# Performance work log

Measured on AMD Instinct MI355X. Metric: run time of the kernel, lower is better.

The kernel has to match this reference:

```python
import jax, jax.numpy as jnp
import numpy as np

NEG_SLOPE = 0.2  # neg_slope init kwarg


def _segment_softmax(logits, seg, n):
    # numerically stable softmax over edges grouped by destination node
    m = jax.ops.segment_max(logits, seg, num_segments=n)          # [N,H]
    e = jnp.exp(logits - m[seg])                                   # [E,H]
    s = jax.ops.segment_sum(e, seg, num_segments=n)                # [N,H]
    return e / (s[seg] + 1e-16)


def _gat_conv(x, src, dst, W, att_src, att_dst, b, n):
    # PyG GATConv (add_self_loops already applied to src/dst), dropout off (eval)
    H, C = att_src.shape
    h = (x @ W).reshape(n, H, C)                                   # [N,H,C]
    a_src = jnp.einsum('nhc,hc->nh', h, att_src)                   # [N,H]
    a_dst = jnp.einsum('nhc,hc->nh', h, att_dst)                   # [N,H]
    logits = jax.nn.leaky_relu(a_src[src] + a_dst[dst], NEG_SLOPE)  # [E,H]
    alpha = _segment_softmax(logits, dst, n)                       # [E,H]
    msg = h[src] * alpha[:, :, None]                               # [E,H,C]
    out = jax.ops.segment_sum(msg, dst, num_segments=n)            # [N,H,C]
    return out.reshape(n, H * C) + b


def setup_inputs() -> dict:
    key = jax.random.key(0)
    ks = jax.random.split(key, 11)
    NU, NI = 10000, 100000
    N = NU + NI
    E = 1_000_000
    IN, HID, HEADS, OUT = 64, 64, 4, 64
    s = 0.1
    return {
        'edge_index': jax.random.randint(ks[0], (2, E), 0, N, dtype=jnp.int64)
            if jax.config.jax_enable_x64 else jax.random.randint(ks[0], (2, E), 0, N),
        'emb_user': jax.random.normal(ks[1], (NU, IN), jnp.float32) * s,
        'emb_item': jax.random.normal(ks[2], (NI, IN), jnp.float32) * s,
        'W1': jax.random.normal(ks[3], (IN, HEADS * HID), jnp.float32) * s,
        'att_src1': jax.random.normal(ks[4], (HEADS, HID), jnp.float32) * s,
        'att_dst1': jax.random.normal(ks[5], (HEADS, HID), jnp.float32) * s,
        'b1': jnp.zeros((HEADS * HID,), jnp.float32),
        'W2': jax.random.normal(ks[6], (HEADS * HID, OUT), jnp.float32) * s,
        'att_src2': jax.random.normal(ks[7], (1, OUT), jnp.float32) * s,
        'att_dst2': jax.random.normal(ks[8], (1, OUT), jnp.float32) * s,
        'b2': jnp.zeros((OUT,), jnp.float32),
    }


def reference(edge_index, emb_user, emb_item, W1, att_src1, att_dst1, b1,
              W2, att_src2, att_dst2, b2):
    NU = emb_user.shape[0]
    N = NU + emb_item.shape[0]
    x = jnp.concatenate([emb_user, emb_item], axis=0)              # [N,IN]
    # GATConv adds self-loops by default
    loops = jnp.arange(N, dtype=edge_index.dtype)
    src = jnp.concatenate([edge_index[0], loops])
    dst = jnp.concatenate([edge_index[1], loops])
    # dropout layers are identity in eval mode
    x = _gat_conv(x, src, dst, W1, att_src1, att_dst1, b1, N)      # [N,HEADS*HID]
    x = jax.nn.elu(x)
    x = _gat_conv(x, src, dst, W2, att_src2, att_dst2, b2, N)      # [N,OUT]
    return x[:NU], x[NU:]
```

## Files before the change

kernel.cpp:

```cpp
#include <hip/hip_runtime.h>
#include <math.h>


typedef float f32x4 __attribute__((ext_vector_type(4)));
typedef short s16x8 __attribute__((ext_vector_type(8)));

#define CHUNK 4096
#define CAPB 6400
#define PADM 1536
#define CAPT (CAPB + PADM)
#define G2PAD 264

static __device__ __forceinline__ short f2bf(float f) {
    unsigned u = __builtin_bit_cast(unsigned, f);
    u = (u + 0x7fff + ((u >> 16) & 1)) >> 16;
    return (short)u;
}
static __device__ __forceinline__ float bf2f(unsigned short u) {
    unsigned v = ((unsigned)u) << 16;
    return __builtin_bit_cast(float, v);
}


__global__ __launch_bounds__(256) void bin_kernel(
    const int* __restrict__ ei, int E, int ET, int* __restrict__ acur,
    unsigned long long* __restrict__ staging) {
    __shared__ unsigned long long eds[CHUNK];
    __shared__ int cnt[256], delta[256], cur[256];
    int t = threadIdx.x;
    cnt[t] = 0;
    __syncthreads();
    int c0 = blockIdx.x * CHUNK;
#pragma unroll
    for (int i = t; i < CHUNK; i += 256) {
        int e = c0 + i;
        unsigned long long v = ~0ull;
        if (e < ET) {
            int s, d;
            if (e < E) { s = ei[e]; d = ei[E + e]; } else { s = e - E; d = e - E; }
            v = ((unsigned long long)(unsigned)d << 32) | (unsigned)s;
            atomicAdd(&cnt[d >> 9], 1);
        }
        eds[i] = v;
    }
    __syncthreads();
    if (t < 64) {
        int loc[4], run = 0;
#pragma unroll
        for (int j = 0; j < 4; ++j) { int v = cnt[t * 4 + j]; loc[j] = run; run += v; }
        int inc = run;
#pragma unroll
        for (int off = 1; off < 64; off <<= 1) {
            int u = __shfl_up(inc, off);
            if (t >= off) inc += u;
        }
        int excl = inc - run;
#pragma unroll
        for (int j = 0; j < 4; ++j) {
            int b = t * 4 + j;
            int lofs = excl + loc[j];
            int c = cnt[b];
            int g = (c > 0) ? atomicAdd(&acur[b], c) : 0;
            delta[b] = b * CAPB + g - lofs;
            cur[b] = lofs;
        }
    }
    __syncthreads();
    for (int i = t; i < CHUNK; i += 256) {
        unsigned long long v = eds[i];
        if (v == ~0ull) continue;
        int b = (int)(v >> 32) >> 9;
        int p = atomicAdd(&cur[b], 1);
        int idx = delta[b] + p;
        if (idx < (b + 1) * CAPB) staging[idx] = v;
    }
}

__global__ __launch_bounds__(256) void bucket_scan_kernel(
    const int* __restrict__ acur, int* __restrict__ bbase, int NB) {
    __shared__ int sc[256];
    int t = threadIdx.x;
    int v = 0;
    if (t < NB) {
        int c = min(acur[t], CAPB);
        v = ((c + 3) & ~3) + PADM;
    }
    sc[t] = v;
    __syncthreads();
    if (t == 0) {
        int run = 0;
        for (int i = 0; i < NB; ++i) { int x = sc[i]; sc[i] = run; run += x; }
    }
    __syncthreads();
    if (t < NB) bbase[t] = sc[t];
}

__global__ __launch_bounds__(256) void bucket_build_kernel(
    const unsigned long long* __restrict__ staging, const int* __restrict__ acur,
    const int* __restrict__ bbase, const float* __restrict__ as1e,
    const float* __restrict__ ad1e, int* __restrict__ offs, int* __restrict__ ends,
    int* __restrict__ csr, int* __restrict__ dstA, float* __restrict__ wts1T,
    int N, int ETp, int NB) {
    __shared__ int src_s[CAPT];
    __shared__ unsigned short ln_s[CAPT];
    __shared__ float adl[512 * 8];
    __shared__ int cnt[512];
    __shared__ int lofs[512];
    __shared__ int tot4_s;
    int b = blockIdx.x;
    int t = threadIdx.x;
    int n0 = b << 9;
    int nn = min(512, N - n0);
    int tot = min(acur[b], CAPB);
    for (int i = t; i < nn * 8; i += 256) adl[i] = ad1e[(size_t)n0 * 8 + i];
    for (int i = t; i < 512; i += 256) cnt[i] = 0;
    for (int i = t; i < CAPT; i += 256) src_s[i] = -1;
    __syncthreads();
    const unsigned long long* sp = staging + (size_t)b * CAPB;
    for (int i = t; i < tot; i += 256)
        atomicAdd(&cnt[(int)(sp[i] >> 32) - n0], 1);
    __syncthreads();
    if (t < 64) {
        int loc[8];
        int run = 0;
#pragma unroll
        for (int j = 0; j < 8; ++j) {
            int v = (cnt[t * 8 + j] + 3) & ~3;
            loc[j] = run;
            run += v;
        }
        int inc = run;
#pragma unroll
        for (int off = 1; off < 64; off <<= 1) {
            int u = __shfl_up(inc, off);
            if (t >= off) inc += u;
        }
        int excl = inc - run;
#pragma unroll
        for (int j = 0; j < 8; ++j) lofs[t * 8 + j] = excl + loc[j];
        if (t == 63) tot4_s = inc;
    }
    __syncthreads();
    int base = bbase[b];
    int tot4 = tot4_s;
    for (int i = t; i < nn; i += 256) {
        int beg = base + lofs[i];
        offs[n0 + i] = beg;
        ends[n0 + i] = beg + ((cnt[i] + 3) & ~3);
    }
    if (b == NB - 1 && t == 0) offs[N] = base + tot4;
    __syncthreads();
    for (int i = t; i < 512; i += 256) cnt[i] = 0;
    __syncthreads();
    for (int i = t; i < tot; i += 256) {
        unsigned long long v = sp[i];
        int s = (int)(v & 0xffffffffu);
        int ln = (int)(v >> 32) - n0;
        int p = lofs[ln] + atomicAdd(&cnt[ln], 1);
        src_s[p] = s;
        ln_s[p] = (unsigned short)ln;
    }
    __syncthreads();
    for (int i = t; i < tot4; i += 256) {
        int s = src_s[i];
        if (s < 0) {
            csr[base + i] = 0;
            dstA[base + i] = -1;
            wts1T[(size_t)0 * ETp + base + i] = 0.f;
            wts1T[(size_t)1 * ETp + base + i] = 0.f;
            wts1T[(size_t)2 * ETp + base + i] = 0.f;
            wts1T[(size_t)3 * ETp + base + i] = 0.f;
        } else {
            int ln = ln_s[i];
            csr[base + i] = s;
            dstA[base + i] = n0 + ln;
            const float4* ap = reinterpret_cast<const float4*>(as1e + (size_t)s * 8);
            float4 a0 = ap[0], a1 = ap[1];
            const float* dl = adl + ln * 8;
            float wA, wB;
            wA = a0.x * dl[0]; wB = a0.y * dl[1];
            wts1T[(size_t)0 * ETp + base + i] = (wA >= 1.f) ? wA : wB;
            wA = a0.z * dl[2]; wB = a0.w * dl[3];
            wts1T[(size_t)1 * ETp + base + i] = (wA >= 1.f) ? wA : wB;
            wA = a1.x * dl[4]; wB = a1.y * dl[5];
            wts1T[(size_t)2 * ETp + base + i] = (wA >= 1.f) ? wA : wB;
            wA = a1.z * dl[6]; wB = a1.w * dl[7];
            wts1T[(size_t)3 * ETp + base + i] = (wA >= 1.f) ? wA : wB;
        }
    }
}

__global__ void edge_w2_kernel(const int* __restrict__ csr,
                               const int* __restrict__ dstA,
                               const float* __restrict__ as2e,
                               const float* __restrict__ ad2e,
                               float* __restrict__ wts2, int ETp) {
    int p = blockIdx.x * blockDim.x + threadIdx.x;
    if (p >= ETp) return;
    int d = dstA[p];
    if (d < 0) { wts2[p] = 0.f; return; }
    int s = csr[p];
    float2 ae = *reinterpret_cast<const float2*>(as2e + (size_t)s * 2);
    float2 de = *reinterpret_cast<const float2*>(ad2e + (size_t)d * 2);
    float wA = ae.x * de.x, wB = ae.y * de.y;
    wts2[p] = (wA >= 1.f) ? wA : wB;
}

__global__ void prep_attv_kernel(const float* __restrict__ W1,
                                 const float* __restrict__ attS1,
                                 const float* __restrict__ attD1,
                                 const float* __restrict__ W2,
                                 const float* __restrict__ attS2,
                                 const float* __restrict__ attD2,
                                 float* __restrict__ attv1s, float* __restrict__ attv1d,
                                 float* __restrict__ attv2s, float* __restrict__ attv2d) {
    int t = threadIdx.x;
    {
        int k = t >> 2, h = t & 3;
        float ss = 0.f, sd = 0.f;
        for (int c = 0; c < 64; ++c) {
            float w = W1[k * 256 + h * 64 + c];
            ss += w * attS1[h * 64 + c];
            sd += w * attD1[h * 64 + c];
        }
        attv1s[k * 4 + h] = ss;
        attv1d[k * 4 + h] = sd;
    }
    {
        float ss = 0.f, sd = 0.f;
        for (int c = 0; c < 64; ++c) {
            float w = W2[t * 64 + c];
            ss += w * attS2[c];
            sd += w * attD2[c];
        }
        attv2s[t] = ss;
        attv2d[t] = sd;
    }
}

__global__ __launch_bounds__(256) void cast_att_kernel(
    const float* __restrict__ xu, const float* __restrict__ xi, int NU, int N,
    const float* __restrict__ attv1s, const float* __restrict__ attv1d,
    unsigned short* __restrict__ xb, float* __restrict__ as1e,
    float* __restrict__ ad1e) {
    int t = threadIdx.x;
    int wv = t >> 6, l = t & 63, l15 = l & 15, lg = l >> 4;

    s16x8 Bfr[2];
#pragma unroll
    for (int ks = 0; ks < 2; ++ks) {
        s16x8 f;
#pragma unroll
        for (int j = 0; j < 8; ++j) {
            int k = ks * 32 + lg * 8 + j;
            float v = 0.f;
            if (l15 < 4) v = attv1s[k * 4 + l15];
            else if (l15 < 8) v = attv1d[k * 4 + (l15 - 4)];
            f[j] = f2bf(v);
        }
        Bfr[ks] = f;
    }

    int ntile = (N + 15) >> 4;
    int wid = blockIdx.x * 4 + wv;
    int stride = gridDim.x * 4;
    for (int tile = wid; tile < ntile; tile += stride) {
        int rbase = tile * 16;
        int arow = rbase + l15;
        bool valid = (arow < N);
        if (!valid) arow = N - 1;
        const float* xp = (arow < NU) ? (xu + (size_t)arow * 64)
                                      : (xi + (size_t)(arow - NU) * 64);
        s16x8 Afr[2];
#pragma unroll
        for (int ks = 0; ks < 2; ++ks) {
            const float4* p = reinterpret_cast<const float4*>(xp + ks * 32 + lg * 8);
            float4 v0 = p[0];
            float4 v1 = p[1];
            s16x8 f;
            f[0] = f2bf(v0.x); f[1] = f2bf(v0.y); f[2] = f2bf(v0.z); f[3] = f2bf(v0.w);
            f[4] = f2bf(v1.x); f[5] = f2bf(v1.y); f[6] = f2bf(v1.z); f[7] = f2bf(v1.w);
            Afr[ks] = f;
            if (valid)
                *reinterpret_cast<s16x8*>(xb + (size_t)arow * 64 + ks * 32 + lg * 8) = f;
        }
        f32x4 acc = (f32x4){0.f, 0.f, 0.f, 0.f};
        acc = __builtin_amdgcn_mfma_f32_16x16x32_bf16(Afr[0], Bfr[0], acc, 0, 0, 0);
        acc = __builtin_amdgcn_mfma_f32_16x16x32_bf16(Afr[1], Bfr[1], acc, 0, 0, 0);
        if (l15 < 8) {
            float* dst = (l15 < 4) ? as1e : ad1e;
            int h = l15 & 3;
#pragma unroll
            for (int i = 0; i < 4; ++i) {
                int r = rbase + lg * 4 + i;
                if (r < N) {
                    float s = acc[i];
                    dst[(size_t)r * 8 + h * 2 + 0] = __expf(s);
                    dst[(size_t)r * 8 + h * 2 + 1] = __expf(0.2f * s);
                }
            }
        }
    }
}

__global__ __launch_bounds__(256) void agg1_kernel(
    const unsigned short* __restrict__ xb, const float* __restrict__ wts1T,
    const int* __restrict__ offs, const int* __restrict__ ends,
    const int* __restrict__ csr, unsigned short* __restrict__ yb, int N, int ETp) {
    int wv = threadIdx.x >> 6, lane = threadIdx.x & 63;
    int n = __builtin_amdgcn_readfirstlane(blockIdx.x * 4 + wv);
    if (n >= N) return;
    int h = lane >> 4, c4 = (lane & 15) * 4;
    int beg = offs[n], end = ends[n];
    const float* wp = wts1T + (size_t)h * ETp;
    float ss = 0.f, a0 = 0.f, a1 = 0.f, a2 = 0.f, a3 = 0.f;

    f32x4 wC = *reinterpret_cast<const f32x4*>(wp + beg);
    ushort4 rC[4];
#pragma unroll
    for (int j = 0; j < 4; ++j) {
        int sj = __builtin_amdgcn_readfirstlane(csr[beg + j]);
        rC[j] = *reinterpret_cast<const ushort4*>(xb + (size_t)sj * 64 + c4);
    }
    for (int o = beg; o < end; o += 4) {
        int oN = o + 4;
        f32x4 wNv;
        ushort4 rN[4];
        if (oN < end) {
            wNv = *reinterpret_cast<const f32x4*>(wp + oN);
#pragma unroll
            for (int j = 0; j < 4; ++j) {
                int sj = __builtin_amdgcn_readfirstlane(csr[oN + j]);
                rN[j] = *reinterpret_cast<const ushort4*>(xb + (size_t)sj * 64 + c4);
            }
        }
#pragma unroll
        for (int j = 0; j < 4; ++j) {
            float w = wC[j];
            ss += w;
            a0 += w * bf2f(rC[j].x);
            a1 += w * bf2f(rC[j].y);
            a2 += w * bf2f(rC[j].z);
            a3 += w * bf2f(rC[j].w);
        }
        wC = wNv;
#pragma unroll
        for (int j = 0; j < 4; ++j) rC[j] = rN[j];
    }
    float inv = 1.f / (ss + 1e-16f);
    ushort4 ov;
    ov.x = (unsigned short)f2bf(a0 * inv);
    ov.y = (unsigned short)f2bf(a1 * inv);
    ov.z = (unsigned short)f2bf(a2 * inv);
    ov.w = (unsigned short)f2bf(a3 * inv);
    *reinterpret_cast<ushort4*>(yb + (size_t)n * 256 + h * 64 + c4) = ov;
}

__global__ __launch_bounds__(256) void gemm_mid_mfma(
    const unsigned short* __restrict__ yb, int N, const float* __restrict__ W1,
    const float* __restrict__ b1, const float* __restrict__ attv2s,
    const float* __restrict__ attv2d, unsigned short* __restrict__ x2,
    float* __restrict__ as2e, float* __restrict__ ad2e) {
    __shared__ float part_s[16][4];
    __shared__ float part_d[16][4];
    int t = threadIdx.x;
    int wv = t >> 6;
    int l = t & 63;
    int l15 = l & 15;
    int lg = l >> 4;

    s16x8 Bfr[4][2];
#pragma unroll
    for (int c = 0; c < 4; ++c)
#pragma unroll
        for (int ks = 0; ks < 2; ++ks) {
            s16x8 f;
#pragma unroll
            for (int j = 0; j < 8; ++j)
                f[j] = f2bf(W1[(size_t)(ks * 32 + lg * 8 + j) * 256 + (wv * 4 + c) * 16 + l15]);
            Bfr[c][ks] = f;
        }
    float bv[4], avs[4], avd[4];
#pragma unroll
    for (int c = 0; c < 4; ++c) {
        int col = (wv * 4 + c) * 16 + l15;
        bv[c] = b1[col];
        avs[c] = attv2s[col];
        avd[c] = attv2d[col];
    }

    int ntile = (N + 15) >> 4;
    for (int tile = blockIdx.x; tile < ntile; tile += gridDim.x) {
        int rbase = tile * 16;
        int arow = rbase + l15;
        if (arow >= N) arow = N - 1;
        const unsigned short* yp = yb + (size_t)arow * 256 + wv * 64;
        s16x8 Afr0 = *reinterpret_cast<const s16x8*>(yp + lg * 8);
        s16x8 Afr1 = *reinterpret_cast<const s16x8*>(yp + 32 + lg * 8);
        f32x4 acc[4];
#pragma unroll
        for (int c = 0; c < 4; ++c) acc[c] = (f32x4){0.f, 0.f, 0.f, 0.f};
#pragma unroll
        for (int c = 0; c < 4; ++c) {
            acc[c] = __builtin_amdgcn_mfma_f32_16x16x32_bf16(Afr0, Bfr[c][0], acc[c], 0, 0, 0);
            acc[c] = __builtin_amdgcn_mfma_f32_16x16x32_bf16(Afr1, Bfr[c][1], acc[c], 0, 0, 0);
        }
        int r0 = rbase + lg * 4;
        float rs[4] = {0.f, 0.f, 0.f, 0.f};
        float rd[4] = {0.f, 0.f, 0.f, 0.f};
#pragma unroll
        for (int c = 0; c < 4; ++c) {
            int col = (wv * 4 + c) * 16 + l15;
#pragma unroll
            for (int i = 0; i < 4; ++i) {
                float v = acc[c][i] + bv[c];
                v = (v > 0.f) ? v : __expf(v) - 1.f;
                rs[i] += v * avs[c];
                rd[i] += v * avd[c];
                int r = r0 + i;
                if (r < N)
                    x2[(size_t)r * 256 + col] = (unsigned short)f2bf(v);
            }
        }
#pragma unroll
        for (int i = 0; i < 4; ++i) {
#pragma unroll
            for (int msk = 8; msk; msk >>= 1) {
                rs[i] += __shfl_xor(rs[i], msk);
                rd[i] += __shfl_xor(rd[i], msk);
            }
            if (l15 == 0) {
                part_s[lg * 4 + i][wv] = rs[i];
                part_d[lg * 4 + i][wv] = rd[i];
            }
        }
        __syncthreads();
        if (t < 16) {
            int r = rbase + t;
            if (r < N) {
                float s = part_s[t][0] + part_s[t][1] + part_s[t][2] + part_s[t][3];
                float d = part_d[t][0] + part_d[t][1] + part_d[t][2] + part_d[t][3];
                as2e[(size_t)r * 2 + 0] = __expf(s);
                as2e[(size_t)r * 2 + 1] = __expf(0.2f * s);
                ad2e[(size_t)r * 2 + 0] = __expf(d);
                ad2e[(size_t)r * 2 + 1] = __expf(0.2f * d);
            }
        }
        __syncthreads();
    }
}

__global__ __launch_bounds__(256) void gemm2_mfma(
    const unsigned short* __restrict__ x2, int N, const float* __restrict__ W2,
    unsigned short* __restrict__ h2) {
    __shared__ unsigned short at[16 * G2PAD];
    int t = threadIdx.x;
    int wv = t >> 6;
    int l = t & 63;
    int l15 = l & 15;
    int lg = l >> 4;

    s16x8 Bfr[8];
#pragma unroll
    for (int ks = 0; ks < 8; ++ks) {
        s16x8 f;
#pragma unroll
        for (int j = 0; j < 8; ++j)
            f[j] = f2bf(W2[(size_t)(ks * 32 + lg * 8 + j) * 64 + wv * 16 + l15]);
        Bfr[ks] = f;
    }

    int ntile = (N + 15) >> 4;
    for (int tile = blockIdx.x; tile < ntile; tile += gridDim.x) {
        int rbase = tile * 16;
        __syncthreads();
#pragma unroll
        for (int k = 0; k < 2; ++k) {
            int i = t * 2 + k;
            int row = i >> 5, c8 = i & 31;
            int r = rbase + row;
            if (r >= N) r = N - 1;
            *reinterpret_cast<uint4*>(at + row * G2PAD + c8 * 8) =
                *reinterpret_cast<const uint4*>(x2 + (size_t)r * 256 + c8 * 8);
        }
        __syncthreads();
        f32x4 acc = (f32x4){0.f, 0.f, 0.f, 0.f};
#pragma unroll
        for (int ks = 0; ks < 8; ++ks) {
            s16x8 Afr = *reinterpret_cast<const s16x8*>(at + l15 * G2PAD + ks * 32 + lg * 8);
            acc = __builtin_amdgcn_mfma_f32_16x16x32_bf16(Afr, Bfr[ks], acc, 0, 0, 0);
        }
        int r0 = rbase + lg * 4;
#pragma unroll
        for (int i = 0; i < 4; ++i) {
            int r = r0 + i;
            if (r < N)
                h2[(size_t)r * 64 + wv * 16 + l15] = (unsigned short)f2bf(acc[i]);
        }
    }
}

__global__ __launch_bounds__(256) void agg2_kernel(
    const unsigned short* __restrict__ h2, const float* __restrict__ wts2,
    const int* __restrict__ offs, const int* __restrict__ ends,
    const int* __restrict__ csr, const float* __restrict__ b2,
    float* __restrict__ out, int N) {
    int wv = threadIdx.x >> 6, lane = threadIdx.x & 63;
    int n = __builtin_amdgcn_readfirstlane(blockIdx.x * 4 + wv);
    if (n >= N) return;
    int beg = offs[n], end = ends[n];
    float ss = 0.f, acc = 0.f;

    f32x4 wC = *reinterpret_cast<const f32x4*>(wts2 + beg);
    unsigned short rC[4];
#pragma unroll
    for (int j = 0; j < 4; ++j) {
        int sj = __builtin_amdgcn_readfirstlane(csr[beg + j]);
        rC[j] = h2[(size_t)sj * 64 + lane];
    }
    for (int o = beg; o < end; o += 4) {
        int oN = o + 4;
        f32x4 wNv;
        unsigned short rN[4];
        if (oN < end) {
            wNv = *reinterpret_cast<const f32x4*>(wts2 + oN);
#pragma unroll
            for (int j = 0; j < 4; ++j) {
                int sj = __builtin_amdgcn_readfirstlane(csr[oN + j]);
                rN[j] = h2[(size_t)sj * 64 + lane];
            }
        }
#pragma unroll
        for (int j = 0; j < 4; ++j) {
            float w = wC[j];
            ss += w;
            acc += w * bf2f(rC[j]);
        }
        wC = wNv;
#pragma unroll
        for (int j = 0; j < 4; ++j) rC[j] = rN[j];
    }
    out[(size_t)n * 64 + lane] = acc / (ss + 1e-16f) + b2[lane];
}


extern "C" void kernel_launch(void* const* d_in, const int* in_sizes, int n_in,
                              void* d_out, int out_size, void* d_ws, size_t ws_size,
                              hipStream_t stream) {
    const int* ei = (const int*)d_in[0];
    const float* xu = (const float*)d_in[1];
    const float* xi = (const float*)d_in[2];
    const float* W1 = (const float*)d_in[3];
    const float* attS1 = (const float*)d_in[4];
    const float* attD1 = (const float*)d_in[5];
    const float* b1 = (const float*)d_in[6];
    const float* W2 = (const float*)d_in[7];
    const float* attS2 = (const float*)d_in[8];
    const float* attD2 = (const float*)d_in[9];
    const float* b2 = (const float*)d_in[10];
    float* out = (float*)d_out;

    const int E = in_sizes[0] / 2;
    const int NU = in_sizes[1] / 64;
    const int NI = in_sizes[2] / 64;
    const int N = NU + NI;
    const int ET = E + N;
    const int NB = (N + 511) >> 9;
    const int ETp = NB * CAPT;

    char* p = (char*)d_ws;
    auto carve = [&](size_t bytes) {
        void* r = (void*)p;
        p += (bytes + 255) & ~(size_t)255;
        return r;
    };
    unsigned short* xb = (unsigned short*)carve((size_t)N * 64 * 2);
    unsigned short* yb = (unsigned short*)carve((size_t)N * 256 * 2);
    unsigned short* x2 = (unsigned short*)carve((size_t)N * 256 * 2);
    float* as1e = (float*)carve((size_t)N * 8 * 4);
    float* ad1e = (float*)carve((size_t)N * 8 * 4);
    float* as2e = (float*)carve((size_t)N * 2 * 4);
    float* ad2e = (float*)carve((size_t)N * 2 * 4);
    float* attv1s = (float*)carve(256 * 4);
    float* attv1d = (float*)carve(256 * 4);
    float* attv2s = (float*)carve(256 * 4);
    float* attv2d = (float*)carve(256 * 4);
    int* offs = (int*)carve((size_t)(N + 1) * 4);
    int* ends = (int*)carve((size_t)N * 4);
    int* csr = (int*)carve((size_t)ETp * 4);
    int* dstA = (int*)carve((size_t)ETp * 4);
    float* wts1T = (float*)carve((size_t)4 * ETp * 4);
    float* wts2 = (float*)carve((size_t)ETp * 4);
    int* acur = (int*)carve((size_t)NB * 4);
    int* bbase = (int*)carve((size_t)NB * 4);
    unsigned long long* staging = (unsigned long long*)yb;
    unsigned short* h2 = yb;

    prep_attv_kernel<<<1, 256, 0, stream>>>(W1, attS1, attD1, W2, attS2, attD2,
                                            attv1s, attv1d, attv2s, attv2d);
    {
        int ntile = (N + 15) >> 4;
        cast_att_kernel<<<(ntile + 3) / 4, 256, 0, stream>>>(
            xu, xi, NU, N, attv1s, attv1d, xb, as1e, ad1e);
    }

    hipMemsetAsync(acur, 0, (size_t)NB * 4, stream);
    hipMemsetAsync(dstA, 0xFF, (size_t)ETp * 4, stream);
    {
        int grid = (ET + CHUNK - 1) / CHUNK;
        bin_kernel<<<grid, 256, 0, stream>>>(ei, E, ET, acur, staging);
    }
    bucket_scan_kernel<<<1, 256, 0, stream>>>(acur, bbase, NB);
    bucket_build_kernel<<<NB, 256, 0, stream>>>(staging, acur, bbase, as1e, ad1e,
                                                offs, ends, csr, dstA, wts1T,
                                                N, ETp, NB);

    agg1_kernel<<<(N + 3) / 4, 256, 0, stream>>>(xb, wts1T, offs, ends, csr, yb, N, ETp);
    gemm_mid_mfma<<<1024, 256, 0, stream>>>(yb, N, W1, b1, attv2s, attv2d, x2, as2e, ad2e);

    {
        int grid = (ETp + 255) / 256;
        edge_w2_kernel<<<grid, 256, 0, stream>>>(csr, dstA, as2e, ad2e, wts2, ETp);
    }
    gemm2_mfma<<<1024, 256, 0, stream>>>(x2, N, W2, h2);
    agg2_kernel<<<(N + 3) / 4, 256, 0, stream>>>(h2, wts2, offs, ends, csr, b2, out, N);
}
```

Baseline: 233.9 us.

## Deepen gather prefetch, drop shared staging in binning, and skip dstA memset

```diff
diff --git a/kernel.cpp b/kernel.cpp
--- a/kernel.cpp
+++ b/kernel.cpp
@@ -5,11 +5,12 @@
 typedef float f32x4 __attribute__((ext_vector_type(4)));
 typedef short s16x8 __attribute__((ext_vector_type(8)));
 
-#define CHUNK 4096
+#define CHUNK 2048
 #define CAPB 6400
 #define PADM 1536
 #define CAPT (CAPB + PADM)
 #define G2PAD 264
+#define SMASK 131071
 
 static __device__ __forceinline__ short f2bf(float f) {
     unsigned u = __builtin_bit_cast(unsigned, f);
@@ -25,23 +26,15 @@
 __global__ __launch_bounds__(256) void bin_kernel(
     const int* __restrict__ ei, int E, int ET, int* __restrict__ acur,
     unsigned long long* __restrict__ staging) {
-    __shared__ unsigned long long eds[CHUNK];
     __shared__ int cnt[256], delta[256], cur[256];
     int t = threadIdx.x;
     cnt[t] = 0;
     __syncthreads();
     int c0 = blockIdx.x * CHUNK;
-#pragma unroll
-    for (int i = t; i < CHUNK; i += 256) {
-        int e = c0 + i;
-        unsigned long long v = ~0ull;
-        if (e < ET) {
-            int s, d;
-            if (e < E) { s = ei[e]; d = ei[E + e]; } else { s = e - E; d = e - E; }
-            v = ((unsigned long long)(unsigned)d << 32) | (unsigned)s;
-            atomicAdd(&cnt[d >> 9], 1);
-        }
-        eds[i] = v;
+    int cend = min(c0 + CHUNK, ET);
+    for (int e = c0 + t; e < cend; e += 256) {
+        int d = (e < E) ? ei[E + e] : (e - E);
+        atomicAdd(&cnt[d >> 9], 1);
     }
     __syncthreads();
     if (t < 64) {
@@ -66,10 +59,11 @@
         }
     }
     __syncthreads();
-    for (int i = t; i < CHUNK; i += 256) {
-        unsigned long long v = eds[i];
-        if (v == ~0ull) continue;
-        int b = (int)(v >> 32) >> 9;
+    for (int e = c0 + t; e < cend; e += 256) {
+        int s, d;
+        if (e < E) { s = ei[e]; d = ei[E + e]; } else { s = e - E; d = e - E; }
+        unsigned long long v = ((unsigned long long)(unsigned)d << 32) | (unsigned)s;
+        int b = d >> 9;
         int p = atomicAdd(&cur[b], 1);
         int idx = delta[b] + p;
         if (idx < (b + 1) * CAPB) staging[idx] = v;
@@ -194,12 +188,15 @@
                                const int* __restrict__ dstA,
                                const float* __restrict__ as2e,
                                const float* __restrict__ ad2e,
-                               float* __restrict__ wts2, int ETp) {
+                               float* __restrict__ wts2, int ETp, int N) {
     int p = blockIdx.x * blockDim.x + threadIdx.x;
     if (p >= ETp) return;
     int d = dstA[p];
-    if (d < 0) { wts2[p] = 0.f; return; }
     int s = csr[p];
+    if ((unsigned)d >= (unsigned)N || (unsigned)s >= (unsigned)N) {
+        wts2[p] = 0.f;
+        return;
+    }
     float2 ae = *reinterpret_cast<const float2*>(as2e + (size_t)s * 2);
     float2 de = *reinterpret_cast<const float2*>(ad2e + (size_t)d * 2);
     float wA = ae.x * de.x, wB = ae.y * de.y;
@@ -315,38 +312,45 @@
     const float* wp = wts1T + (size_t)h * ETp;
     float ss = 0.f, a0 = 0.f, a1 = 0.f, a2 = 0.f, a3 = 0.f;
 
-    f32x4 wC = *reinterpret_cast<const f32x4*>(wp + beg);
-    ushort4 rC[4];
-#pragma unroll
-    for (int j = 0; j < 4; ++j) {
-        int sj = __builtin_amdgcn_readfirstlane(csr[beg + j]);
-        rC[j] = *reinterpret_cast<const ushort4*>(xb + (size_t)sj * 64 + c4);
-    }
-    for (int o = beg; o < end; o += 4) {
-        int oN = o + 4;
-        f32x4 wNv;
-        ushort4 rN[4];
-        if (oN < end) {
-            wNv = *reinterpret_cast<const f32x4*>(wp + oN);
-#pragma unroll
-            for (int j = 0; j < 4; ++j) {
-                int sj = __builtin_amdgcn_readfirstlane(csr[oN + j]);
-                rN[j] = *reinterpret_cast<const ushort4*>(xb + (size_t)sj * 64 + c4);
-            }
-        }
-#pragma unroll
-        for (int j = 0; j < 4; ++j) {
-            float w = wC[j];
-            ss += w;
-            a0 += w * bf2f(rC[j].x);
-            a1 += w * bf2f(rC[j].y);
-            a2 += w * bf2f(rC[j].z);
-            a3 += w * bf2f(rC[j].w);
-        }
-        wC = wNv;
-#pragma unroll
-        for (int j = 0; j < 4; ++j) rC[j] = rN[j];
-    }
+    f32x4 w0, w1, w2;
+    ushort4 r0[4], r1[4], r2[4];
+
+#define A1_LOAD(W, R, O)                                                          \
+    {                                                                             \
+        W = *reinterpret_cast<const f32x4*>(wp + (O));                            \
+        _Pragma("unroll") for (int j = 0; j < 4; ++j) {                           \
+            int sj = __builtin_amdgcn_readfirstlane(csr[(O) + j]) & SMASK;        \
+            R[j] = *reinterpret_cast<const ushort4*>(xb + (size_t)sj * 64 + c4);  \
+        }                                                                         \
+    }
+#define A1_PROC(W, R)                                                            \
+    {                                                                            \
+        _Pragma("unroll") for (int j = 0; j < 4; ++j) {                          \
+            float w = W[j];                                                      \
+            ss += w;                                                             \
+            a0 += w * bf2f(R[j].x);                                             \
+            a1 += w * bf2f(R[j].y);                                             \
+            a2 += w * bf2f(R[j].z);                                             \
+            a3 += w * bf2f(R[j].w);                                             \
+        }                                                                        \
+    }
+
+    A1_LOAD(w0, r0, beg)
+    A1_LOAD(w1, r1, beg + 4)
+    int o = beg;
+    while (true) {
+        if (o + 8 < end) A1_LOAD(w2, r2, o + 8)
+        A1_PROC(w0, r0)
+        o += 4; if (o >= end) break;
+        if (o + 8 < end) A1_LOAD(w0, r0, o + 8)
+        A1_PROC(w1, r1)
+        o += 4; if (o >= end) break;
+        if (o + 8 < end) A1_LOAD(w1, r1, o + 8)
+        A1_PROC(w2, r2)
+        o += 4; if (o >= end) break;
+    }
+#undef A1_LOAD
+#undef A1_PROC
     float inv = 1.f / (ss + 1e-16f);
     ushort4 ov;
     ov.x = (unsigned short)f2bf(a0 * inv);
@@ -511,35 +515,42 @@
     int beg = offs[n], end = ends[n];
     float ss = 0.f, acc = 0.f;
 
-    f32x4 wC = *reinterpret_cast<const f32x4*>(wts2 + beg);
-    unsigned short rC[4];
-#pragma unroll
-    for (int j = 0; j < 4; ++j) {
-        int sj = __builtin_amdgcn_readfirstlane(csr[beg + j]);
-        rC[j] = h2[(size_t)sj * 64 + lane];
-    }
-    for (int o = beg; o < end; o += 4) {
-        int oN = o + 4;
-        f32x4 wNv;
-        unsigned short rN[4];
-        if (oN < end) {
-            wNv = *reinterpret_cast<const f32x4*>(wts2 + oN);
-#pragma unroll
-            for (int j = 0; j < 4; ++j) {
-                int sj = __builtin_amdgcn_readfirstlane(csr[oN + j]);
-                rN[j] = h2[(size_t)sj * 64 + lane];
-            }
-        }
-#pragma unroll
-        for (int j = 0; j < 4; ++j) {
-            float w = wC[j];
-            ss += w;
-            acc += w * bf2f(rC[j]);
-        }
-        wC = wNv;
-#pragma unroll
-        for (int j = 0; j < 4; ++j) rC[j] = rN[j];
-    }
+    f32x4 w0, w1, w2;
+    unsigned short r0[4], r1[4], r2[4];
+
+#define A2_LOAD(W, R, O)                                                   \
+    {                                                                      \
+        W = *reinterpret_cast<const f32x4*>(wts2 + (O));                   \
+        _Pragma("unroll") for (int j = 0; j < 4; ++j) {                    \
+            int sj = __builtin_amdgcn_readfirstlane(csr[(O) + j]) & SMASK; \
+            R[j] = h2[(size_t)sj * 64 + lane];                             \
+        }                                                                  \
+    }
+#define A2_PROC(W, R)                                                      \
+    {                                                                      \
+        _Pragma("unroll") for (int j = 0; j < 4; ++j) {                    \
+            float w = W[j];                                                \
+            ss += w;                                                       \
+            acc += w * bf2f(R[j]);                                         \
+        }                                                                  \
+    }
+
+    A2_LOAD(w0, r0, beg)
+    A2_LOAD(w1, r1, beg + 4)
+    int o = beg;
+    while (true) {
+        if (o + 8 < end) A2_LOAD(w2, r2, o + 8)
+        A2_PROC(w0, r0)
+        o += 4; if (o >= end) break;
+        if (o + 8 < end) A2_LOAD(w0, r0, o + 8)
+        A2_PROC(w1, r1)
+        o += 4; if (o >= end) break;
+        if (o + 8 < end) A2_LOAD(w1, r1, o + 8)
+        A2_PROC(w2, r2)
+        o += 4; if (o >= end) break;
+    }
+#undef A2_LOAD
+#undef A2_PROC
     out[(size_t)n * 64 + lane] = acc / (ss + 1e-16f) + b2[lane];
 }
 
@@ -590,7 +601,7 @@
     int* csr = (int*)carve((size_t)ETp * 4);
     int* dstA = (int*)carve((size_t)ETp * 4);
     float* wts1T = (float*)carve((size_t)4 * ETp * 4);
-    float* wts2 = (float*)carve((size_t)ETp * 4);
+    float* wts2 = (float*)carve(((size_t)ETp + 16) * 4);
     int* acur = (int*)carve((size_t)NB * 4);
     int* bbase = (int*)carve((size_t)NB * 4);
     unsigned long long* staging = (unsigned long long*)yb;
@@ -605,7 +616,6 @@
     }
 
     hipMemsetAsync(acur, 0, (size_t)NB * 4, stream);
-    hipMemsetAsync(dstA, 0xFF, (size_t)ETp * 4, stream);
     {
         int grid = (ET + CHUNK - 1) / CHUNK;
         bin_kernel<<<grid, 256, 0, stream>>>(ei, E, ET, acur, staging);
@@ -620,7 +630,7 @@
 
     {
         int grid = (ETp + 255) / 256;
-        edge_w2_kernel<<<grid, 256, 0, stream>>>(csr, dstA, as2e, ad2e, wts2, ETp);
+        edge_w2_kernel<<<grid, 256, 0, stream>>>(csr, dstA, as2e, ad2e, wts2, ETp, N);
     }
     gemm2_mfma<<<1024, 256, 0, stream>>>(x2, N, W2, h2);
     agg2_kernel<<<(N + 3) / 4, 256, 0, stream>>>(h2, wts2, offs, ends, csr, b2, out, N);
```

After: 243.3 us. 4.0% more time.
